# Kernel tuning notes

Measured on AMD Instinct MI355X. Metric: run time of the kernel, lower is better.

## Reference

```python
import jax, jax.numpy as jnp
import numpy as np

# Config (mirrors CorrLayerDownsample(J=3, L=8, A=1, A_prime=1, M=256, N=256,
# num_channels=1, shift_mode='samec', mask_angles=4)). With samec + 1 channel,
# every pair is 'shifted' (mask index 1) and groups (j1,j2) are contiguous in
# the global moment order, so concatenation reproduces results_storage order.
J, L, A, M, N, NB = 3, 8, 1, 256, 256, 2
MASK_ANGLES = 4
RADII = (1, 2)  # dyadic shift radii (assumed form of create_masks_shift)

def _mask_positions():
    # shift mask 1: origin plus shifts along mask_angles directions at dyadic radii
    pos = {(0, 0)}
    for k in range(MASK_ANGLES):
        th = np.pi * k / MASK_ANGLES
        for r in RADII:
            pos.add((int(round(r * np.cos(th))), int(round(r * np.sin(th)))))
    return sorted(pos)

def _union_flat_idx(h, w):
    # row-major flat indices of the union shift mask at resolution (h, w),
    # matching torch boolean-mask indexing order (mask_downsample + mask_idx_map_1)
    return np.array(sorted(((dx % h) * w + (dy % w)) for dx, dy in _mask_positions()), dtype=np.int64)

UNION_IDX = [_union_flat_idx(M >> j, N >> j) for j in range(J)]
NSHIFT = len(UNION_IDX[0])

# per-(j1,j2) channel gather indices: la = A*L*c + A*l + a = l (A=1, c=0)
# loop order in compute_idx: l1 outer, l2 inner
LA1 = np.repeat(np.arange(L), L)
LA2 = np.tile(np.arange(L), L)

def _spectral_pad(xh, Mn, Nn):
    # zero-pad Fourier representation to (Mn, Nn) -- spectral upsampling
    m, n = xh.shape[-2], xh.shape[-1]
    if (m, n) == (Mn, Nn):
        return xh
    xs = jnp.fft.fftshift(xh, axes=(-2, -1))
    ph, pw = (Mn - m) // 2, (Nn - n) // 2
    pad = [(0, 0)] * (xh.ndim - 2) + [(ph, ph), (pw, pw)]
    xp = jnp.pad(xs, pad)
    return jnp.fft.ifftshift(xp, axes=(-2, -1)) * ((Mn * Nn) / (m * n))

def _forward(xpsi_0, xpsi_1, xpsi_2):
    xs = [xpsi_0, xpsi_1, xpsi_2]
    hats = [jnp.fft.fft2(x.astype(jnp.complex64)) for x in xs]  # [nb, C, h_j, w_j]
    la1 = jnp.asarray(LA1)
    la2 = jnp.asarray(LA2)
    outs = []
    for j1 in range(J):
        h, w = M >> j1, N >> j1
        uidx = jnp.asarray(UNION_IDX[j1])
        h1 = hats[j1][:, la1]  # [nb, P=L*L, h, w]
        for j2 in range(j1, J):
            h2 = hats[j2][:, la2]
            if j2 > j1:
                h2 = _spectral_pad(h2, h, w)  # upsample coarser scale to scale j1
            corr = jnp.fft.ifft2(h1 * jnp.conj(h2)).real  # cross-correlation map
            flat = corr.reshape(corr.shape[0], corr.shape[1], h * w)
            outs.append(flat[:, :, uidx])  # masked downsample: keep shift positions
    return jnp.concatenate(outs, axis=1)  # [nb, total_pairs, NSHIFT]

def setup_inputs():
    key = jax.random.key(0)
    ks = jax.random.split(key, 3)
    return {
        "xpsi_0": jax.random.normal(ks[0], (NB, A * L, M, N), dtype=jnp.float32),
        "xpsi_1": jax.random.normal(ks[1], (NB, A * L, M // 2, N // 2), dtype=jnp.float32),
        "xpsi_2": jax.random.normal(ks[2], (NB, A * L, M // 4, N // 4), dtype=jnp.float32),
    }

def reference(xpsi_0, xpsi_1, xpsi_2):
    return _forward(xpsi_0, xpsi_1, xpsi_2)
```

## Files before the change

### kernel.cpp

```cpp
#include <hip/hip_runtime.h>

#define PI_D 3.14159265358979323846
#define PI_F 3.14159265358979323846f


__device__ inline float rtab_val(int n, int m2, int t) {
  if (t == 0) return 1.0f;
  double th = PI_D * (double)t / (double)n;
  double v = sin(th * (double)(m2 - 1)) / sin(th) + cos(th * (double)m2);
  return (float)(v / (double)m2);
}

__global__ __launch_bounds__(256) void k_front(const float* __restrict__ X1,
                                               const float* __restrict__ X2,
                                               float* __restrict__ P1p,
                                               float* __restrict__ P2p,
                                               float* __restrict__ V01,
                                               float* __restrict__ V02,
                                               float* __restrict__ V12,
                                               float* __restrict__ out) {
  int bid = blockIdx.x;
  int t = threadIdx.x;
  if (bid == 640) {
    for (int i = t; i < 5376; i += 256) out[i] = 0.f;
    return;
  }
  if (bid < 192) {
    const float* X; float* P; int lg, nsp, idx0;
    if (bid < 128) { X = X1; P = P1p; lg = 7; nsp = 8; idx0 = bid; }
    else           { X = X2; P = P2p; lg = 6; nsp = 4; idx0 = bid - 128; }
    int ch = idx0 / nsp, split = idx0 % nsp;
    int n = 1 << lg;
    int total = n * n;
    int chunk = total / nsp;
    int b0 = split * chunk;
    const float* x = X + (size_t)ch * total + b0;
    float s = 0.f;
    for (int i = t; i < chunk; i += 256) {
      int idx = b0 + i;
      float v = x[i];
      s += (((idx >> lg) ^ idx) & 1) ? -v : v;
    }
#pragma unroll
    for (int off = 32; off > 0; off >>= 1) s += __shfl_down(s, off, 64);
    __shared__ float red[4];
    if ((t & 63) == 0) red[t >> 6] = s;
    __syncthreads();
    if (t == 0) P[ch * nsp + split] = red[0] + red[1] + red[2] + red[3];
    return;
  }
  int vbid = bid - 192;
  const float* X; float* V;
  int n1, n2, s, ch, nxg, colh;
  if (vbid < 256) {
    X = X1; V = V01; n1 = 256; n2 = 128; s = 2;
    ch = vbid >> 4; nxg = ((vbid >> 1) & 7) * 16; colh = vbid & 1;
  } else if (vbid < 384) {
    int w = vbid - 256;
    X = X2; V = V02; n1 = 256; n2 = 64; s = 4;
    ch = w >> 3; nxg = ((w >> 1) & 3) * 16; colh = w & 1;
  } else {
    int w = vbid - 384;
    X = X2; V = V12; n1 = 128; n2 = 64; s = 2;
    ch = w >> 2; nxg = (w & 3) * 16; colh = 0;
  }
  __shared__ float Rl[256];
  __shared__ float Xs[16 * 128];
  for (int i = t; i < n1; i += 256) Rl[i] = rtab_val(n1, n2, i);
  const float4* xch4 =
      (const float4*)(X + (size_t)ch * n2 * n2 + (size_t)nxg * n2);
  int nx4 = (16 * n2) >> 2;
  for (int i = t; i < nx4; i += 256) ((float4*)Xs)[i] = xch4[i];
  __syncthreads();
  int myq = (t & 63) + colh * 128;
  int nxq = t >> 6;
  int mask = n1 - 1;
  float acc[4][2];
#pragma unroll
  for (int r = 0; r < 4; ++r)
#pragma unroll
    for (int c = 0; c < 2; ++c) acc[r][c] = 0.f;
  for (int ny = 0; ny < n2; ++ny) {
    float xv[4];
#pragma unroll
    for (int r = 0; r < 4; ++r) xv[r] = Xs[(4 * nxq + r) * n2 + ny];
#pragma unroll
    for (int c = 0; c < 2; ++c) {
      float rv = Rl[(myq + 64 * c - s * ny) & mask];
#pragma unroll
      for (int r = 0; r < 4; ++r) acc[r][c] += xv[r] * rv;
    }
  }
  float* vch = V + (size_t)ch * n2 * n1;
#pragma unroll
  for (int r = 0; r < 4; ++r)
    for (int c = 0; c < 2; ++c)
      vch[(size_t)(nxg + 4 * nxq + r) * n1 + myq + 64 * c] = acc[r][c];
}

__global__ __launch_bounds__(256) void k_main(const float* __restrict__ X0,
                                              const float* __restrict__ X1,
                                              const float* __restrict__ X2,
                                              const float* __restrict__ V01,
                                              const float* __restrict__ V02,
                                              const float* __restrict__ V12,
                                              const float* __restrict__ P1p,
                                              const float* __restrict__ P2p,
                                              float* __restrict__ out) {
  __shared__ float sRl[256];
  __shared__ float4 R4[256];
  __shared__ float sh[4864];
  int u = blockIdx.x;
  int t = threadIdx.x;
  int lane = t & 63;
  int wv = t >> 6;

  float accC[8][7];
#pragma unroll
  for (int i = 0; i < 8; ++i)
#pragma unroll
    for (int p = 0; p < 7; ++p) accC[i][p] = 0.f;

  int base, b, l2;

  if (u < 640) {
    const float* V; const float* Pp; const float* A1b;
    int n1, n2, s, ch, chunk, nsp, lgn1; float inv;
    if (u < 256)      { V = V01; Pp = P1p; nsp = 8; A1b = X0; n1 = 256; n2 = 128; s = 2; inv = 1.f / (128.f * 128.f); ch = u >> 4; chunk = u & 15; lgn1 = 8; base = 64; }
    else if (u < 512) { int w = u - 256; V = V02; Pp = P2p; nsp = 4; A1b = X0; n1 = 256; n2 = 64; s = 4; inv = 1.f / (64.f * 64.f); ch = w >> 4; chunk = w & 15; lgn1 = 8; base = 128; }
    else              { int w = u - 512; V = V12; Pp = P2p; nsp = 4; A1b = X1; n1 = 128; n2 = 64; s = 2; inv = 1.f / (64.f * 64.f); ch = w >> 3; chunk = w & 7; lgn1 = 7; base = 256; }
    int mask = n1 - 1;
    for (int i = t; i < n1; i += 256) sRl[i] = rtab_val(n1, n2, i);
    __syncthreads();
    for (int i = t; i < n1; i += 256)
      R4[i] = make_float4(sRl[i], sRl[(i + 1) & mask], sRl[(i + 2) & mask],
                          sRl[(i + 3) & mask]);
    __syncthreads();
    int mxg = chunk * 16;
    b = ch >> 3; l2 = ch & 7;
    const float* vch = V + (size_t)ch * n2 * n1;
    float Pv = 0.f;
    for (int i = 0; i < nsp; ++i) Pv += Pp[ch * nsp + i];
    float a = PI_F / (float)s;
    int per = 2 * s;
    if (n1 == 256) {
      int cid = t & 63;
      int rb = mxg - 2 + 5 * wv;
      float4 acc[5];
#pragma unroll
      for (int j = 0; j < 5; ++j) acc[j] = make_float4(0.f, 0.f, 0.f, 0.f);
      float4 vv = *(const float4*)(vch + 4 * cid);
      for (int nx = 0; nx < n2; ++nx) {
        float4 vvn;
        if (nx + 1 < n2) vvn = *(const float4*)(vch + (size_t)(nx + 1) * 256 + 4 * cid);
        int ib = (rb - s * nx) & mask;
        float4 r03 = R4[ib];
        float r4v = sRl[(ib + 4) & mask];
        float rv[5] = {r03.x, r03.y, r03.z, r03.w, r4v};
#pragma unroll
        for (int j = 0; j < 5; ++j) {
          acc[j].x += rv[j] * vv.x; acc[j].y += rv[j] * vv.y;
          acc[j].z += rv[j] * vv.z; acc[j].w += rv[j] * vv.w;
        }
        vv = vvn;
      }
      float smy[4];
#pragma unroll
      for (int j = 0; j < 4; ++j) smy[j] = sinf(a * (float)((4 * cid + j) & (per - 1)));
#pragma unroll
      for (int j = 0; j < 5; ++j) {
        int rl = 5 * wv + j;
        if (rl < 19) {
          int mx = (mxg - 2 + rl) & mask;
          float q = inv * sinf(a * (float)(mx & (per - 1))) * Pv;
          float4 o = acc[j];
          o.x -= q * smy[0]; o.y -= q * smy[1]; o.z -= q * smy[2]; o.w -= q * smy[3];
          *(float4*)&sh[rl * 256 + 4 * cid] = o;
        }
      }
    } else {
      int cid = t & 31;
      int owner = t >> 5;
      int rb = mxg - 2 + 3 * owner;
      float4 acc[3];
#pragma unroll
      for (int j = 0; j < 3; ++j) acc[j] = make_float4(0.f, 0.f, 0.f, 0.f);
      float4 vv = *(const float4*)(vch + 4 * cid);
      for (int nx = 0; nx < 64; ++nx) {
        float4 vvn;
        if (nx + 1 < 64) vvn = *(const float4*)(vch + (size_t)(nx + 1) * 128 + 4 * cid);
        int ib = (rb - 2 * nx) & 127;
        float4 r03 = R4[ib];
        float rv[3] = {r03.x, r03.y, r03.z};
#pragma unroll
        for (int j = 0; j < 3; ++j) {
          acc[j].x += rv[j] * vv.x; acc[j].y += rv[j] * vv.y;
          acc[j].z += rv[j] * vv.z; acc[j].w += rv[j] * vv.w;
        }
        vv = vvn;
      }
      float smy[4];
#pragma unroll
      for (int j = 0; j < 4; ++j) smy[j] = sinf(a * (float)((4 * cid + j) & 3));
#pragma unroll
      for (int j = 0; j < 3; ++j) {
        int rl = 3 * owner + j;
        if (rl < 19) {
          int mx = (mxg - 2 + rl) & 127;
          float q = inv * sinf(a * (float)(mx & 3)) * Pv;
          float4 o = acc[j];
          o.x -= q * smy[0]; o.y -= q * smy[1]; o.z -= q * smy[2]; o.w -= q * smy[3];
          *(float4*)&sh[rl * 128 + 4 * cid] = o;
        }
      }
    }
    __syncthreads();
    int lgtpr = lgn1 - 2;
    int tpr = 1 << lgtpr;
    int rif = 256 >> lgtpr;
    int rid = t >> lgtpr;
    int cid2 = t & (tpr - 1);
    int ty = cid2 * 4;
    int tym = (ty - 4) & mask;
    int n1sq = n1 * n1;
    const float* A1 = A1b + (size_t)(b * 8) * n1sq;
    for (int rr = 0; rr < 16; rr += rif) {
      int ri = rr + rid;
      const float* r0 = &sh[(ri + 2) * n1];
      const float* r1 = &sh[(ri + 1) * n1];
      const float* r2 = &sh[ri * n1];
      const float* r3 = &sh[(ri + 3) * n1];
      float4 a0 = *(const float4*)(r0 + tym);
      float4 b0 = *(const float4*)(r0 + ty);
      float4 a1 = *(const float4*)(r1 + tym);
      float4 b1 = *(const float4*)(r1 + ty);
      float4 b2 = *(const float4*)(r2 + ty);
      float4 a3 = *(const float4*)(r3 + tym);
      float4 b3 = *(const float4*)(r3 + ty);
      const float* rA = A1 + (size_t)(mxg + ri) * n1 + ty;
#pragma unroll
      for (int l1 = 0; l1 < 8; ++l1) {
        float4 xv = *(const float4*)(rA + (size_t)l1 * n1sq);
        accC[l1][0] += xv.x * b0.x + xv.y * b0.y + xv.z * b0.z + xv.w * b0.w;
        accC[l1][1] += xv.x * a0.w + xv.y * b0.x + xv.z * b0.y + xv.w * b0.z;
        accC[l1][2] += xv.x * a0.z + xv.y * a0.w + xv.z * b0.x + xv.w * b0.y;
        accC[l1][3] += xv.x * b1.x + xv.y * b1.y + xv.z * b1.z + xv.w * b1.w;
        accC[l1][4] += xv.x * a1.w + xv.y * b1.x + xv.z * b1.y + xv.w * b1.z;
        accC[l1][5] += xv.x * b2.x + xv.y * b2.y + xv.z * b2.z + xv.w * b2.w;
        accC[l1][6] += xv.x * a3.w + xv.y * b3.x + xv.z * b3.y + xv.w * b3.z;
      }
    }
  } else {
    int w = u - 640;
    const float* Ab; int loc, lgn1, lgc;
    if (w < 256)      { loc = w;       Ab = X0; lgn1 = 8; lgc = 4; base = 0;   }
    else if (w < 384) { loc = w - 256; Ab = X1; lgn1 = 7; lgc = 3; base = 192; }
    else              { loc = w - 384; Ab = X2; lgn1 = 6; lgc = 2; base = 320; }
    int n1 = 1 << lgn1;
    int mask = n1 - 1;
    int n1sq = n1 * n1;
    int chunk = loc & ((1 << lgc) - 1);
    int bl2 = loc >> lgc;
    b = bl2 >> 3; l2 = bl2 & 7;
    const float* A1 = Ab + (size_t)(b * 8) * n1sq;
    const float* A2 = Ab + (size_t)(b * 8 + l2) * n1sq;
    int lgtpr = lgn1 - 2;
    int tpr = 1 << lgtpr;
    int rif = 256 >> lgtpr;
    int rid = t >> lgtpr;
    int cid2 = t & (tpr - 1);
    int ty = cid2 * 4;
    int tym = (ty - 4) & mask;
    for (int rr = 0; rr < 16; rr += rif) {
      int row = chunk * 16 + rr + rid;
      const float* r0 = A2 + (size_t)row * n1;
      const float* r1 = A2 + (size_t)((row - 1) & mask) * n1;
      const float* r2 = A2 + (size_t)((row - 2) & mask) * n1;
      const float* r3 = A2 + (size_t)((row + 1) & mask) * n1;
      float4 a0 = *(const float4*)(r0 + tym);
      float4 b0 = *(const float4*)(r0 + ty);
      float4 a1 = *(const float4*)(r1 + tym);
      float4 b1 = *(const float4*)(r1 + ty);
      float4 b2 = *(const float4*)(r2 + ty);
      float4 a3 = *(const float4*)(r3 + tym);
      float4 b3 = *(const float4*)(r3 + ty);
      const float* rA = A1 + (size_t)row * n1 + ty;
#pragma unroll
      for (int l1 = 0; l1 < 8; ++l1) {
        float4 xv = *(const float4*)(rA + (size_t)l1 * n1sq);
        accC[l1][0] += xv.x * b0.x + xv.y * b0.y + xv.z * b0.z + xv.w * b0.w;
        accC[l1][1] += xv.x * a0.w + xv.y * b0.x + xv.z * b0.y + xv.w * b0.z;
        accC[l1][2] += xv.x * a0.z + xv.y * a0.w + xv.z * b0.x + xv.w * b0.y;
        accC[l1][3] += xv.x * b1.x + xv.y * b1.y + xv.z * b1.z + xv.w * b1.w;
        accC[l1][4] += xv.x * a1.w + xv.y * b1.x + xv.z * b1.y + xv.w * b1.z;
        accC[l1][5] += xv.x * b2.x + xv.y * b2.y + xv.z * b2.z + xv.w * b2.w;
        accC[l1][6] += xv.x * a3.w + xv.y * b3.x + xv.z * b3.y + xv.w * b3.z;
      }
    }
  }
  float* af = &accC[0][0];
#pragma unroll
  for (int j = 0; j < 56; ++j) {
    float v = af[j];
    v += __shfl_down(v, 32, 64);
    v += __shfl_down(v, 16, 64);
    af[j] = v;
  }
  __syncthreads();
  if (lane < 16) {
    float* rowp = sh + (wv * 16 + lane) * 60;
#pragma unroll
    for (int j = 0; j < 14; ++j)
      *(float4*)&rowp[4 * j] =
          make_float4(af[4 * j], af[4 * j + 1], af[4 * j + 2], af[4 * j + 3]);
  }
  __syncthreads();
  if (t < 224) {
    int v = t >> 2, q = t & 3;
    float s2 = 0.f;
#pragma unroll
    for (int i = 0; i < 16; ++i) s2 += sh[(q * 16 + i) * 60 + v];
    s2 += __shfl_down(s2, 2, 64);
    s2 += __shfl_down(s2, 1, 64);
    if (q == 0) {
      int l1o = v / 7, p = v % 7;
      atomicAdd(&out[((size_t)b * 384 + base + l1o * 8 + l2) * 7 + p], s2);
    }
  }
}

extern "C" void kernel_launch(void* const* d_in, const int* in_sizes, int n_in,
                              void* d_out, int out_size, void* d_ws, size_t ws_size,
                              hipStream_t stream) {
  const float* X0 = (const float*)d_in[0];
  const float* X1 = (const float*)d_in[1];
  const float* X2 = (const float*)d_in[2];
  float* out = (float*)d_out;
  float* ws = (float*)d_ws;

  float* V01 = ws + 2359296;
  float* V02 = ws + 2883584;
  float* V12 = ws + 3145728;
  float* P1p = ws + 3276800;
  float* P2p = ws + 3276928;

  k_front<<<641, 256, 0, stream>>>(X1, X2, P1p, P2p, V01, V02, V12, out);
  k_main<<<1088, 256, 0, stream>>>(X0, X1, X2, V01, V02, V12, P1p, P2p, out);
}
```

Measured before the change: 102.7 us.

## Skip interpolation on exact-sample rows, move same-scale blocks to front kernel

The upsampling table is now computed in float with reduced-argument sin/cos instead of double precision. Rows and columns whose upsampled positions land on original samples are copied straight from the coarse input instead of being computed by the interpolation sum, and only the remaining rows are interpolated. The 448 same-scale correlation blocks move from the main kernel into the front kernel so they run concurrently with the V-table construction, and output zeroing becomes a memset. The risks are float accuracy in the table and uneven work across waves.

After: 96.56 us. 1.06x faster.

```diff
diff --git a/kernel.cpp b/kernel.cpp
--- a/kernel.cpp
+++ b/kernel.cpp
@@ -1,30 +1,115 @@
 #include <hip/hip_runtime.h>
 
-#define PI_D 3.14159265358979323846
 #define PI_F 3.14159265358979323846f
 
 
-__device__ inline float rtab_val(int n, int m2, int t) {
+__device__ __forceinline__ float rtab_f(int n, int m2, int t) {
   if (t == 0) return 1.0f;
-  double th = PI_D * (double)t / (double)n;
-  double v = sin(th * (double)(m2 - 1)) / sin(th) + cos(th * (double)m2);
-  return (float)(v / (double)m2);
-}
-
-__global__ __launch_bounds__(256) void k_front(const float* __restrict__ X1,
-                                               const float* __restrict__ X2,
-                                               float* __restrict__ P1p,
-                                               float* __restrict__ P2p,
-                                               float* __restrict__ V01,
-                                               float* __restrict__ V02,
-                                               float* __restrict__ V12,
-                                               float* __restrict__ out) {
+  int tw = 2 * n - 1;
+  float th = PI_F * (float)t / (float)n;
+  int A = (t * (m2 - 1)) & tw;
+  int B = (t * m2) & tw;
+  float v = sinf(PI_F * (float)A / (float)n) / sinf(th) +
+            cosf(PI_F * (float)B / (float)n);
+  return v / (float)m2;
+}
+
+template <int NR>
+__device__ __forceinline__ void phaseA256(const float* __restrict__ vch,
+                                          const float* __restrict__ sRl,
+                                          float* __restrict__ sh,
+                                          const int (&rls)[NR], int mxg, int s,
+                                          int n2, float inv, float Pv, float a,
+                                          int per, int cid) {
+  int bj[NR];
+#pragma unroll
+  for (int j = 0; j < NR; ++j) bj[j] = (mxg - 2 + rls[j]) & 255;
+  float4 acc[NR];
+#pragma unroll
+  for (int j = 0; j < NR; ++j) acc[j] = make_float4(0.f, 0.f, 0.f, 0.f);
+  const float4* vp = (const float4*)vch + cid;
+  float4 va = vp[0];
+  float4 vb = vp[64];
+  for (int nx = 0; nx < n2; ++nx) {
+    float4 vc = make_float4(0.f, 0.f, 0.f, 0.f);
+    if (nx + 2 < n2) vc = vp[(size_t)(nx + 2) * 64];
+    int ss = s * nx;
+#pragma unroll
+    for (int j = 0; j < NR; ++j) {
+      float rv = sRl[(bj[j] - ss) & 255];
+      acc[j].x += rv * va.x;
+      acc[j].y += rv * va.y;
+      acc[j].z += rv * va.z;
+      acc[j].w += rv * va.w;
+    }
+    va = vb;
+    vb = vc;
+  }
+  float smy[4];
+#pragma unroll
+  for (int j = 0; j < 4; ++j)
+    smy[j] = sinf(a * (float)((4 * cid + j) & (per - 1)));
+#pragma unroll
+  for (int j = 0; j < NR; ++j) {
+    float q = inv * sinf(a * (float)(bj[j] & (per - 1))) * Pv;
+    float4 o = acc[j];
+    o.x -= q * smy[0];
+    o.y -= q * smy[1];
+    o.z -= q * smy[2];
+    o.w -= q * smy[3];
+    *(float4*)&sh[rls[j] * 256 + 4 * cid] = o;
+  }
+}
+
+template <int NR>
+__device__ __forceinline__ void phaseA128(const float* __restrict__ vch,
+                                          const float* __restrict__ sRl,
+                                          float* __restrict__ sh,
+                                          const int (&rls)[NR], int mxg, int n2,
+                                          float inv, float Pv, int cid) {
+  int bj[NR];
+#pragma unroll
+  for (int j = 0; j < NR; ++j) bj[j] = (mxg - 2 + rls[j]) & 127;
+  float2 acc[NR];
+#pragma unroll
+  for (int j = 0; j < NR; ++j) acc[j] = make_float2(0.f, 0.f);
+  const float2* vp = (const float2*)vch + cid;
+  float2 va = vp[0];
+  float2 vb = vp[64];
+  for (int nx = 0; nx < n2; ++nx) {
+    float2 vc = make_float2(0.f, 0.f);
+    if (nx + 2 < n2) vc = vp[(size_t)(nx + 2) * 64];
+    int ss = 2 * nx;
+#pragma unroll
+    for (int j = 0; j < NR; ++j) {
+      float rv = sRl[(bj[j] - ss) & 127];
+      acc[j].x += rv * va.x;
+      acc[j].y += rv * va.y;
+    }
+    va = vb;
+    vb = vc;
+  }
+  const float a = PI_F * 0.5f;
+  float smy0 = sinf(a * (float)((2 * cid) & 3));
+  float smy1 = sinf(a * (float)((2 * cid + 1) & 3));
+#pragma unroll
+  for (int j = 0; j < NR; ++j) {
+    float q = inv * sinf(a * (float)(bj[j] & 3)) * Pv;
+    float2 o = acc[j];
+    o.x -= q * smy0;
+    o.y -= q * smy1;
+    *(float2*)&sh[rls[j] * 128 + 2 * cid] = o;
+  }
+}
+
+__global__ __launch_bounds__(256) void k_front(
+    const float* __restrict__ X0, const float* __restrict__ X1,
+    const float* __restrict__ X2, float* __restrict__ P1p,
+    float* __restrict__ P2p, float* __restrict__ V01, float* __restrict__ V02,
+    float* __restrict__ V12, float* __restrict__ out) {
+  __shared__ float fsm[4864];
   int bid = blockIdx.x;
   int t = threadIdx.x;
-  if (bid == 640) {
-    for (int i = t; i < 5376; i += 256) out[i] = 0.f;
-    return;
-  }
   if (bid < 192) {
     const float* X; float* P; int lg, nsp, idx0;
     if (bid < 128) { X = X1; P = P1p; lg = 7; nsp = 8; idx0 = bid; }
@@ -49,58 +134,176 @@
     if (t == 0) P[ch * nsp + split] = red[0] + red[1] + red[2] + red[3];
     return;
   }
-  int vbid = bid - 192;
-  const float* X; float* V;
-  int n1, n2, s, ch, nxg, colh;
-  if (vbid < 256) {
-    X = X1; V = V01; n1 = 256; n2 = 128; s = 2;
-    ch = vbid >> 4; nxg = ((vbid >> 1) & 7) * 16; colh = vbid & 1;
-  } else if (vbid < 384) {
-    int w = vbid - 256;
-    X = X2; V = V02; n1 = 256; n2 = 64; s = 4;
-    ch = w >> 3; nxg = ((w >> 1) & 3) * 16; colh = w & 1;
-  } else {
-    int w = vbid - 384;
-    X = X2; V = V12; n1 = 128; n2 = 64; s = 2;
-    ch = w >> 2; nxg = (w & 3) * 16; colh = 0;
-  }
-  __shared__ float Rl[256];
-  __shared__ float Xs[16 * 128];
-  for (int i = t; i < n1; i += 256) Rl[i] = rtab_val(n1, n2, i);
-  const float4* xch4 =
-      (const float4*)(X + (size_t)ch * n2 * n2 + (size_t)nxg * n2);
-  int nx4 = (16 * n2) >> 2;
-  for (int i = t; i < nx4; i += 256) ((float4*)Xs)[i] = xch4[i];
-  __syncthreads();
-  int myq = (t & 63) + colh * 128;
-  int nxq = t >> 6;
+  if (bid < 320) {
+    int idx = bid - 192;
+    int ch = idx >> 3, nxg = (idx & 7) * 16;
+    float* Rl = fsm;
+    float* Xs = fsm + 256;
+    for (int i = t; i < 256; i += 256) Rl[i] = rtab_f(256, 128, i);
+    const float4* xch4 =
+        (const float4*)(X1 + (size_t)ch * 16384 + (size_t)nxg * 128);
+    for (int i = t; i < 512; i += 256) ((float4*)Xs)[i] = xch4[i];
+    __syncthreads();
+    float* vch = V01 + (size_t)ch * 128 * 256;
+    for (int i = t; i < 2048; i += 256) {
+      int r = i >> 7, k = i & 127;
+      vch[(size_t)(nxg + r) * 256 + 2 * k] = Xs[r * 128 + k];
+    }
+    int cid = t & 63, wq = t >> 6;
+    int m0 = 2 * cid + 1, m1 = 2 * cid + 129;
+    float acc[4][2];
+#pragma unroll
+    for (int r = 0; r < 4; ++r) { acc[r][0] = 0.f; acc[r][1] = 0.f; }
+    for (int ny = 0; ny < 128; ++ny) {
+      float r0 = Rl[(m0 - 2 * ny) & 255];
+      float r1 = Rl[(m1 - 2 * ny) & 255];
+#pragma unroll
+      for (int r = 0; r < 4; ++r) {
+        float xv = Xs[(4 * wq + r) * 128 + ny];
+        acc[r][0] += xv * r0;
+        acc[r][1] += xv * r1;
+      }
+    }
+#pragma unroll
+    for (int r = 0; r < 4; ++r) {
+      vch[(size_t)(nxg + 4 * wq + r) * 256 + m0] = acc[r][0];
+      vch[(size_t)(nxg + 4 * wq + r) * 256 + m1] = acc[r][1];
+    }
+    return;
+  }
+  if (bid < 512) {
+    int vbid = bid - 320;
+    const float* X = X2; float* V;
+    int n1, n2, s, ch, nxg, colh;
+    if (vbid < 128) {
+      V = V02; n1 = 256; n2 = 64; s = 4;
+      ch = vbid >> 3; nxg = ((vbid >> 1) & 3) * 16; colh = vbid & 1;
+    } else {
+      int w = vbid - 128;
+      V = V12; n1 = 128; n2 = 64; s = 2;
+      ch = w >> 2; nxg = (w & 3) * 16; colh = 0;
+    }
+    float* Rl = fsm;
+    float* Xs = fsm + 256;
+    for (int i = t; i < n1; i += 256) Rl[i] = rtab_f(n1, n2, i);
+    const float4* xch4 =
+        (const float4*)(X + (size_t)ch * n2 * n2 + (size_t)nxg * n2);
+    int nx4 = (16 * n2) >> 2;
+    for (int i = t; i < nx4; i += 256) ((float4*)Xs)[i] = xch4[i];
+    __syncthreads();
+    int myq = (t & 63) + colh * 128;
+    int nxq = t >> 6;
+    int mask = n1 - 1;
+    float acc[4][2];
+#pragma unroll
+    for (int r = 0; r < 4; ++r)
+#pragma unroll
+      for (int c = 0; c < 2; ++c) acc[r][c] = 0.f;
+    for (int ny = 0; ny < n2; ++ny) {
+      float xv[4];
+#pragma unroll
+      for (int r = 0; r < 4; ++r) xv[r] = Xs[(4 * nxq + r) * n2 + ny];
+#pragma unroll
+      for (int c = 0; c < 2; ++c) {
+        float rv = Rl[(myq + 64 * c - s * ny) & mask];
+#pragma unroll
+        for (int r = 0; r < 4; ++r) acc[r][c] += xv[r] * rv;
+      }
+    }
+    float* vch = V + (size_t)ch * n2 * n1;
+#pragma unroll
+    for (int r = 0; r < 4; ++r)
+      for (int c = 0; c < 2; ++c)
+        vch[(size_t)(nxg + 4 * nxq + r) * n1 + myq + 64 * c] = acc[r][c];
+    return;
+  }
+  int lane = t & 63;
+  int wv = t >> 6;
+  float accC[8][7];
+#pragma unroll
+  for (int i = 0; i < 8; ++i)
+#pragma unroll
+    for (int p = 0; p < 7; ++p) accC[i][p] = 0.f;
+  int w = bid - 512;
+  const float* Ab; int loc, lgn1, lgc, base;
+  if (w < 256)      { loc = w;       Ab = X0; lgn1 = 8; lgc = 4; base = 0;   }
+  else if (w < 384) { loc = w - 256; Ab = X1; lgn1 = 7; lgc = 3; base = 192; }
+  else              { loc = w - 384; Ab = X2; lgn1 = 6; lgc = 2; base = 320; }
+  int n1 = 1 << lgn1;
   int mask = n1 - 1;
-  float acc[4][2];
-#pragma unroll
-  for (int r = 0; r < 4; ++r)
-#pragma unroll
-    for (int c = 0; c < 2; ++c) acc[r][c] = 0.f;
-  for (int ny = 0; ny < n2; ++ny) {
-    float xv[4];
-#pragma unroll
-    for (int r = 0; r < 4; ++r) xv[r] = Xs[(4 * nxq + r) * n2 + ny];
-#pragma unroll
-    for (int c = 0; c < 2; ++c) {
-      float rv = Rl[(myq + 64 * c - s * ny) & mask];
-#pragma unroll
-      for (int r = 0; r < 4; ++r) acc[r][c] += xv[r] * rv;
-    }
-  }
-  float* vch = V + (size_t)ch * n2 * n1;
-#pragma unroll
-  for (int r = 0; r < 4; ++r)
-    for (int c = 0; c < 2; ++c)
-      vch[(size_t)(nxg + 4 * nxq + r) * n1 + myq + 64 * c] = acc[r][c];
+  int n1sq = n1 * n1;
+  int chunk = loc & ((1 << lgc) - 1);
+  int bl2 = loc >> lgc;
+  int b = bl2 >> 3, l2 = bl2 & 7;
+  const float* A1 = Ab + (size_t)(b * 8) * n1sq;
+  const float* A2 = Ab + (size_t)(b * 8 + l2) * n1sq;
+  int lgtpr = lgn1 - 2;
+  int tpr = 1 << lgtpr;
+  int rif = 256 >> lgtpr;
+  int rid = t >> lgtpr;
+  int cid2 = t & (tpr - 1);
+  int ty = cid2 * 4;
+  int tym = (ty - 4) & mask;
+  for (int rr = 0; rr < 16; rr += rif) {
+    int row = chunk * 16 + rr + rid;
+    const float* r0 = A2 + (size_t)row * n1;
+    const float* r1 = A2 + (size_t)((row - 1) & mask) * n1;
+    const float* r2 = A2 + (size_t)((row - 2) & mask) * n1;
+    const float* r3 = A2 + (size_t)((row + 1) & mask) * n1;
+    float4 a0 = *(const float4*)(r0 + tym);
+    float4 b0 = *(const float4*)(r0 + ty);
+    float4 a1 = *(const float4*)(r1 + tym);
+    float4 b1 = *(const float4*)(r1 + ty);
+    float4 b2 = *(const float4*)(r2 + ty);
+    float4 a3 = *(const float4*)(r3 + tym);
+    float4 b3 = *(const float4*)(r3 + ty);
+    const float* rA = A1 + (size_t)row * n1 + ty;
+#pragma unroll
+    for (int l1 = 0; l1 < 8; ++l1) {
+      float4 xv = *(const float4*)(rA + (size_t)l1 * n1sq);
+      accC[l1][0] += xv.x * b0.x + xv.y * b0.y + xv.z * b0.z + xv.w * b0.w;
+      accC[l1][1] += xv.x * a0.w + xv.y * b0.x + xv.z * b0.y + xv.w * b0.z;
+      accC[l1][2] += xv.x * a0.z + xv.y * a0.w + xv.z * b0.x + xv.w * b0.y;
+      accC[l1][3] += xv.x * b1.x + xv.y * b1.y + xv.z * b1.z + xv.w * b1.w;
+      accC[l1][4] += xv.x * a1.w + xv.y * b1.x + xv.z * b1.y + xv.w * b1.z;
+      accC[l1][5] += xv.x * b2.x + xv.y * b2.y + xv.z * b2.z + xv.w * b2.w;
+      accC[l1][6] += xv.x * a3.w + xv.y * b3.x + xv.z * b3.y + xv.w * b3.z;
+    }
+  }
+  float* sh = fsm;
+  float* af = &accC[0][0];
+#pragma unroll
+  for (int j = 0; j < 56; ++j) {
+    float v = af[j];
+    v += __shfl_down(v, 32, 64);
+    v += __shfl_down(v, 16, 64);
+    af[j] = v;
+  }
+  __syncthreads();
+  if (lane < 16) {
+    float* rowp = sh + (wv * 16 + lane) * 60;
+#pragma unroll
+    for (int j = 0; j < 14; ++j)
+      *(float4*)&rowp[4 * j] =
+          make_float4(af[4 * j], af[4 * j + 1], af[4 * j + 2], af[4 * j + 3]);
+  }
+  __syncthreads();
+  if (t < 224) {
+    int v = t >> 2, q = t & 3;
+    float s2 = 0.f;
+#pragma unroll
+    for (int i = 0; i < 16; ++i) s2 += sh[(q * 16 + i) * 60 + v];
+    s2 += __shfl_down(s2, 2, 64);
+    s2 += __shfl_down(s2, 1, 64);
+    if (q == 0) {
+      int l1o = v / 7, p = v % 7;
+      atomicAdd(&out[((size_t)b * 384 + base + l1o * 8 + l2) * 7 + p], s2);
+    }
+  }
 }
 
 __global__ __launch_bounds__(256) void k_main(const float* __restrict__ X0,
                                               const float* __restrict__ X1,
-                                              const float* __restrict__ X2,
                                               const float* __restrict__ V01,
                                               const float* __restrict__ V02,
                                               const float* __restrict__ V12,
@@ -108,7 +311,6 @@
                                               const float* __restrict__ P2p,
                                               float* __restrict__ out) {
   __shared__ float sRl[256];
-  __shared__ float4 R4[256];
   __shared__ float sh[4864];
   int u = blockIdx.x;
   int t = threadIdx.x;
@@ -121,183 +323,116 @@
 #pragma unroll
     for (int p = 0; p < 7; ++p) accC[i][p] = 0.f;
 
-  int base, b, l2;
-
-  if (u < 640) {
-    const float* V; const float* Pp; const float* A1b;
-    int n1, n2, s, ch, chunk, nsp, lgn1; float inv;
-    if (u < 256)      { V = V01; Pp = P1p; nsp = 8; A1b = X0; n1 = 256; n2 = 128; s = 2; inv = 1.f / (128.f * 128.f); ch = u >> 4; chunk = u & 15; lgn1 = 8; base = 64; }
-    else if (u < 512) { int w = u - 256; V = V02; Pp = P2p; nsp = 4; A1b = X0; n1 = 256; n2 = 64; s = 4; inv = 1.f / (64.f * 64.f); ch = w >> 4; chunk = w & 15; lgn1 = 8; base = 128; }
-    else              { int w = u - 512; V = V12; Pp = P2p; nsp = 4; A1b = X1; n1 = 128; n2 = 64; s = 2; inv = 1.f / (64.f * 64.f); ch = w >> 3; chunk = w & 7; lgn1 = 7; base = 256; }
-    int mask = n1 - 1;
-    for (int i = t; i < n1; i += 256) sRl[i] = rtab_val(n1, n2, i);
-    __syncthreads();
-    for (int i = t; i < n1; i += 256)
-      R4[i] = make_float4(sRl[i], sRl[(i + 1) & mask], sRl[(i + 2) & mask],
-                          sRl[(i + 3) & mask]);
-    __syncthreads();
-    int mxg = chunk * 16;
-    b = ch >> 3; l2 = ch & 7;
-    const float* vch = V + (size_t)ch * n2 * n1;
-    float Pv = 0.f;
-    for (int i = 0; i < nsp; ++i) Pv += Pp[ch * nsp + i];
-    float a = PI_F / (float)s;
-    int per = 2 * s;
-    if (n1 == 256) {
-      int cid = t & 63;
-      int rb = mxg - 2 + 5 * wv;
-      float4 acc[5];
-#pragma unroll
-      for (int j = 0; j < 5; ++j) acc[j] = make_float4(0.f, 0.f, 0.f, 0.f);
-      float4 vv = *(const float4*)(vch + 4 * cid);
-      for (int nx = 0; nx < n2; ++nx) {
-        float4 vvn;
-        if (nx + 1 < n2) vvn = *(const float4*)(vch + (size_t)(nx + 1) * 256 + 4 * cid);
-        int ib = (rb - s * nx) & mask;
-        float4 r03 = R4[ib];
-        float r4v = sRl[(ib + 4) & mask];
-        float rv[5] = {r03.x, r03.y, r03.z, r03.w, r4v};
-#pragma unroll
-        for (int j = 0; j < 5; ++j) {
-          acc[j].x += rv[j] * vv.x; acc[j].y += rv[j] * vv.y;
-          acc[j].z += rv[j] * vv.z; acc[j].w += rv[j] * vv.w;
+  const float* V; const float* Pp; const float* A1b;
+  int n1, n2, s, ch, chunk, nsp, lgn1, base; float inv;
+  if (u < 256) {
+    V = V01; Pp = P1p; nsp = 8; A1b = X0; n1 = 256; n2 = 128; s = 2;
+    inv = 1.f / 16384.f; ch = u >> 4; chunk = u & 15; lgn1 = 8; base = 64;
+  } else if (u < 512) {
+    int w = u - 256;
+    V = V02; Pp = P2p; nsp = 4; A1b = X0; n1 = 256; n2 = 64; s = 4;
+    inv = 1.f / 4096.f; ch = w >> 4; chunk = w & 15; lgn1 = 8; base = 128;
+  } else {
+    int w = u - 512;
+    V = V12; Pp = P2p; nsp = 4; A1b = X1; n1 = 128; n2 = 64; s = 2;
+    inv = 1.f / 4096.f; ch = w >> 3; chunk = w & 7; lgn1 = 7; base = 256;
+  }
+  int mask = n1 - 1;
+  for (int i = t; i < n1; i += 256) sRl[i] = rtab_f(n1, n2, i);
+  __syncthreads();
+  int mxg = chunk * 16;
+  int b = ch >> 3, l2 = ch & 7;
+  const float* vch = V + (size_t)ch * n2 * n1;
+  float Pv = 0.f;
+  for (int i = 0; i < nsp; ++i) Pv += Pp[ch * nsp + i];
+  float a = PI_F / (float)s;
+  int per = 2 * s;
+
+  if (n1 == 256) {
+    if (s == 2) {
+      if (wv < 3) {
+        int rls[3] = {6 * wv + 1, 6 * wv + 3, 6 * wv + 5};
+        phaseA256<3>(vch, sRl, sh, rls, mxg, 2, 128, inv, Pv, a, per, lane);
+      } else {
+        for (int i = lane; i < 640; i += 64) {
+          int rl = 2 * (i >> 6), c4 = (i & 63) * 4;
+          int mx = (mxg - 2 + rl) & 255;
+          *(float4*)&sh[rl * 256 + c4] =
+              *(const float4*)(vch + (size_t)(mx >> 1) * 256 + c4);
         }
-        vv = vvn;
-      }
-      float smy[4];
-#pragma unroll
-      for (int j = 0; j < 4; ++j) smy[j] = sinf(a * (float)((4 * cid + j) & (per - 1)));
-#pragma unroll
-      for (int j = 0; j < 5; ++j) {
-        int rl = 5 * wv + j;
-        if (rl < 19) {
-          int mx = (mxg - 2 + rl) & mask;
-          float q = inv * sinf(a * (float)(mx & (per - 1))) * Pv;
-          float4 o = acc[j];
-          o.x -= q * smy[0]; o.y -= q * smy[1]; o.z -= q * smy[2]; o.w -= q * smy[3];
-          *(float4*)&sh[rl * 256 + 4 * cid] = o;
-        }
       }
     } else {
-      int cid = t & 31;
-      int owner = t >> 5;
-      int rb = mxg - 2 + 3 * owner;
-      float4 acc[3];
-#pragma unroll
-      for (int j = 0; j < 3; ++j) acc[j] = make_float4(0.f, 0.f, 0.f, 0.f);
-      float4 vv = *(const float4*)(vch + 4 * cid);
-      for (int nx = 0; nx < 64; ++nx) {
-        float4 vvn;
-        if (nx + 1 < 64) vvn = *(const float4*)(vch + (size_t)(nx + 1) * 128 + 4 * cid);
-        int ib = (rb - 2 * nx) & 127;
-        float4 r03 = R4[ib];
-        float rv[3] = {r03.x, r03.y, r03.z};
-#pragma unroll
-        for (int j = 0; j < 3; ++j) {
-          acc[j].x += rv[j] * vv.x; acc[j].y += rv[j] * vv.y;
-          acc[j].z += rv[j] * vv.z; acc[j].w += rv[j] * vv.w;
-        }
-        vv = vvn;
-      }
-      float smy[4];
-#pragma unroll
-      for (int j = 0; j < 4; ++j) smy[j] = sinf(a * (float)((4 * cid + j) & 3));
-#pragma unroll
-      for (int j = 0; j < 3; ++j) {
-        int rl = 3 * owner + j;
-        if (rl < 19) {
-          int mx = (mxg - 2 + rl) & 127;
-          float q = inv * sinf(a * (float)(mx & 3)) * Pv;
-          float4 o = acc[j];
-          o.x -= q * smy[0]; o.y -= q * smy[1]; o.z -= q * smy[2]; o.w -= q * smy[3];
-          *(float4*)&sh[rl * 128 + 4 * cid] = o;
-        }
-      }
-    }
-    __syncthreads();
-    int lgtpr = lgn1 - 2;
-    int tpr = 1 << lgtpr;
-    int rif = 256 >> lgtpr;
-    int rid = t >> lgtpr;
-    int cid2 = t & (tpr - 1);
-    int ty = cid2 * 4;
-    int tym = (ty - 4) & mask;
-    int n1sq = n1 * n1;
-    const float* A1 = A1b + (size_t)(b * 8) * n1sq;
-    for (int rr = 0; rr < 16; rr += rif) {
-      int ri = rr + rid;
-      const float* r0 = &sh[(ri + 2) * n1];
-      const float* r1 = &sh[(ri + 1) * n1];
-      const float* r2 = &sh[ri * n1];
-      const float* r3 = &sh[(ri + 3) * n1];
-      float4 a0 = *(const float4*)(r0 + tym);
-      float4 b0 = *(const float4*)(r0 + ty);
-      float4 a1 = *(const float4*)(r1 + tym);
-      float4 b1 = *(const float4*)(r1 + ty);
-      float4 b2 = *(const float4*)(r2 + ty);
-      float4 a3 = *(const float4*)(r3 + tym);
-      float4 b3 = *(const float4*)(r3 + ty);
-      const float* rA = A1 + (size_t)(mxg + ri) * n1 + ty;
-#pragma unroll
-      for (int l1 = 0; l1 < 8; ++l1) {
-        float4 xv = *(const float4*)(rA + (size_t)l1 * n1sq);
-        accC[l1][0] += xv.x * b0.x + xv.y * b0.y + xv.z * b0.z + xv.w * b0.w;
-        accC[l1][1] += xv.x * a0.w + xv.y * b0.x + xv.z * b0.y + xv.w * b0.z;
-        accC[l1][2] += xv.x * a0.z + xv.y * a0.w + xv.z * b0.x + xv.w * b0.y;
-        accC[l1][3] += xv.x * b1.x + xv.y * b1.y + xv.z * b1.z + xv.w * b1.w;
-        accC[l1][4] += xv.x * a1.w + xv.y * b1.x + xv.z * b1.y + xv.w * b1.z;
-        accC[l1][5] += xv.x * b2.x + xv.y * b2.y + xv.z * b2.z + xv.w * b2.w;
-        accC[l1][6] += xv.x * a3.w + xv.y * b3.x + xv.z * b3.y + xv.w * b3.z;
+      if (wv == 0) {
+        int rls[4] = {0, 1, 3, 4};
+        phaseA256<4>(vch, sRl, sh, rls, mxg, 4, 64, inv, Pv, a, per, lane);
+      } else if (wv == 1) {
+        int rls[4] = {5, 7, 8, 9};
+        phaseA256<4>(vch, sRl, sh, rls, mxg, 4, 64, inv, Pv, a, per, lane);
+      } else if (wv == 2) {
+        int rls[3] = {11, 12, 13};
+        phaseA256<3>(vch, sRl, sh, rls, mxg, 4, 64, inv, Pv, a, per, lane);
+      } else {
+        int rls[3] = {15, 16, 17};
+        phaseA256<3>(vch, sRl, sh, rls, mxg, 4, 64, inv, Pv, a, per, lane);
+      }
+      for (int i = t; i < 320; i += 256) {
+        int rl = 2 + 4 * (i >> 6), c4 = (i & 63) * 4;
+        int mx = (mxg - 2 + rl) & 255;
+        *(float4*)&sh[rl * 256 + c4] =
+            *(const float4*)(vch + (size_t)(mx >> 2) * 256 + c4);
       }
     }
   } else {
-    int w = u - 640;
-    const float* Ab; int loc, lgn1, lgc;
-    if (w < 256)      { loc = w;       Ab = X0; lgn1 = 8; lgc = 4; base = 0;   }
-    else if (w < 384) { loc = w - 256; Ab = X1; lgn1 = 7; lgc = 3; base = 192; }
-    else              { loc = w - 384; Ab = X2; lgn1 = 6; lgc = 2; base = 320; }
-    int n1 = 1 << lgn1;
-    int mask = n1 - 1;
-    int n1sq = n1 * n1;
-    int chunk = loc & ((1 << lgc) - 1);
-    int bl2 = loc >> lgc;
-    b = bl2 >> 3; l2 = bl2 & 7;
-    const float* A1 = Ab + (size_t)(b * 8) * n1sq;
-    const float* A2 = Ab + (size_t)(b * 8 + l2) * n1sq;
-    int lgtpr = lgn1 - 2;
-    int tpr = 1 << lgtpr;
-    int rif = 256 >> lgtpr;
-    int rid = t >> lgtpr;
-    int cid2 = t & (tpr - 1);
-    int ty = cid2 * 4;
-    int tym = (ty - 4) & mask;
-    for (int rr = 0; rr < 16; rr += rif) {
-      int row = chunk * 16 + rr + rid;
-      const float* r0 = A2 + (size_t)row * n1;
-      const float* r1 = A2 + (size_t)((row - 1) & mask) * n1;
-      const float* r2 = A2 + (size_t)((row - 2) & mask) * n1;
-      const float* r3 = A2 + (size_t)((row + 1) & mask) * n1;
-      float4 a0 = *(const float4*)(r0 + tym);
-      float4 b0 = *(const float4*)(r0 + ty);
-      float4 a1 = *(const float4*)(r1 + tym);
-      float4 b1 = *(const float4*)(r1 + ty);
-      float4 b2 = *(const float4*)(r2 + ty);
-      float4 a3 = *(const float4*)(r3 + tym);
-      float4 b3 = *(const float4*)(r3 + ty);
-      const float* rA = A1 + (size_t)row * n1 + ty;
-#pragma unroll
-      for (int l1 = 0; l1 < 8; ++l1) {
-        float4 xv = *(const float4*)(rA + (size_t)l1 * n1sq);
-        accC[l1][0] += xv.x * b0.x + xv.y * b0.y + xv.z * b0.z + xv.w * b0.w;
-        accC[l1][1] += xv.x * a0.w + xv.y * b0.x + xv.z * b0.y + xv.w * b0.z;
-        accC[l1][2] += xv.x * a0.z + xv.y * a0.w + xv.z * b0.x + xv.w * b0.y;
-        accC[l1][3] += xv.x * b1.x + xv.y * b1.y + xv.z * b1.z + xv.w * b1.w;
-        accC[l1][4] += xv.x * a1.w + xv.y * b1.x + xv.z * b1.y + xv.w * b1.z;
-        accC[l1][5] += xv.x * b2.x + xv.y * b2.y + xv.z * b2.z + xv.w * b2.w;
-        accC[l1][6] += xv.x * a3.w + xv.y * b3.x + xv.z * b3.y + xv.w * b3.z;
-      }
-    }
-  }
+    if (wv < 3) {
+      int rls[3] = {6 * wv + 1, 6 * wv + 3, 6 * wv + 5};
+      phaseA128<3>(vch, sRl, sh, rls, mxg, 64, inv, Pv, lane);
+    } else {
+      for (int i = lane; i < 320; i += 64) {
+        int rl = 2 * (i >> 5), c4 = (i & 31) * 4;
+        int mx = (mxg - 2 + rl) & 127;
+        *(float4*)&sh[rl * 128 + c4] =
+            *(const float4*)(vch + (size_t)(mx >> 1) * 128 + c4);
+      }
+    }
+  }
+  __syncthreads();
+
+  int lgtpr = lgn1 - 2;
+  int tpr = 1 << lgtpr;
+  int rif = 256 >> lgtpr;
+  int rid = t >> lgtpr;
+  int cid2 = t & (tpr - 1);
+  int ty = cid2 * 4;
+  int tym = (ty - 4) & mask;
+  int n1sq = n1 * n1;
+  const float* A1 = A1b + (size_t)(b * 8) * n1sq;
+  for (int rr = 0; rr < 16; rr += rif) {
+    int ri = rr + rid;
+    const float* r0 = &sh[(ri + 2) * n1];
+    const float* r1 = &sh[(ri + 1) * n1];
+    const float* r2 = &sh[ri * n1];
+    const float* r3 = &sh[(ri + 3) * n1];
+    float4 a0 = *(const float4*)(r0 + tym);
+    float4 b0 = *(const float4*)(r0 + ty);
+    float4 a1 = *(const float4*)(r1 + tym);
+    float4 b1 = *(const float4*)(r1 + ty);
+    float4 b2 = *(const float4*)(r2 + ty);
+    float4 a3 = *(const float4*)(r3 + tym);
+    float4 b3 = *(const float4*)(r3 + ty);
+    const float* rA = A1 + (size_t)(mxg + ri) * n1 + ty;
+#pragma unroll
+    for (int l1 = 0; l1 < 8; ++l1) {
+      float4 xv = *(const float4*)(rA + (size_t)l1 * n1sq);
+      accC[l1][0] += xv.x * b0.x + xv.y * b0.y + xv.z * b0.z + xv.w * b0.w;
+      accC[l1][1] += xv.x * a0.w + xv.y * b0.x + xv.z * b0.y + xv.w * b0.z;
+      accC[l1][2] += xv.x * a0.z + xv.y * a0.w + xv.z * b0.x + xv.w * b0.y;
+      accC[l1][3] += xv.x * b1.x + xv.y * b1.y + xv.z * b1.z + xv.w * b1.w;
+      accC[l1][4] += xv.x * a1.w + xv.y * b1.x + xv.z * b1.y + xv.w * b1.z;
+      accC[l1][5] += xv.x * b2.x + xv.y * b2.y + xv.z * b2.z + xv.w * b2.w;
+      accC[l1][6] += xv.x * a3.w + xv.y * b3.x + xv.z * b3.y + xv.w * b3.z;
+    }
+  }
+
   float* af = &accC[0][0];
 #pragma unroll
   for (int j = 0; j < 56; ++j) {
@@ -344,6 +479,7 @@
   float* P1p = ws + 3276800;
   float* P2p = ws + 3276928;
 
-  k_front<<<641, 256, 0, stream>>>(X1, X2, P1p, P2p, V01, V02, V12, out);
-  k_main<<<1088, 256, 0, stream>>>(X0, X1, X2, V01, V02, V12, P1p, P2p, out);
-}
+  hipMemsetAsync(d_out, 0, (size_t)out_size, stream);
+  k_front<<<960, 256, 0, stream>>>(X0, X1, X2, P1p, P2p, V01, V02, V12, out);
+  k_main<<<640, 256, 0, stream>>>(X0, X1, V01, V02, V12, P1p, P2p, out);
+}
```
